# Optimization experiments

Measured on AMD Instinct MI355X. Metric: run time of the kernel, lower is better.

Reference implementation:

```python
import jax, jax.numpy as jnp
import numpy as np
from jax import lax

BETA = 0.1

def setup_inputs() -> dict:
    key = jax.random.key(0)
    k = jax.random.split(key, 6)
    B, T, H, V = 2, 1024, 1024, 64000
    return {
        "_input": jax.random.normal(k[0], (B, T, H), jnp.float32) * 0.02,
        "weight": jax.random.normal(k[1], (V, H), jnp.float32) * 0.02,
        "attention_mask": (jax.random.uniform(k[2], (B, T)) < 0.9).astype(jnp.float32),
        "rewards": jax.random.normal(k[3], (B,), jnp.float32),
        "ref_input": jax.random.normal(k[4], (B, T, H), jnp.float32) * 0.02,
        "ref_weight": jax.random.normal(k[5], (V, H), jnp.float32) * 0.02,
    }


def _grpo(log_probs, attention_mask, rewards, ref_log_probs, beta):
    # log_probs: [B,T,V]
    chosen = jnp.argmax(log_probs, axis=-1)  # [B,T] int
    tok_lp = jnp.take_along_axis(log_probs, chosen[..., None], axis=-1)[..., 0]  # [B,T]
    ref_tok_lp = lax.stop_gradient(
        jnp.take_along_axis(ref_log_probs, chosen[..., None], axis=-1)[..., 0]
    )
    adv = (rewards - rewards.mean()) / (jnp.std(rewards, ddof=1) + 1e-8)  # [B]
    ratio = jnp.exp(tok_lp - lax.stop_gradient(tok_lp))  # == 1 in fwd, grad-carrying
    policy_loss = -ratio * adv[:, None]
    d = ref_tok_lp - tok_lp
    kl = jnp.exp(d) - d - 1.0
    per_tok = (policy_loss + beta * kl) * attention_mask
    seqlen = jnp.clip(attention_mask.sum(axis=1), 1.0)
    loss = (per_tok.sum(axis=1) / seqlen).mean()
    metrics = (
        tok_lp.mean(),
        jnp.std(tok_lp, ddof=1),
        log_probs.mean(),
        (kl * attention_mask).sum(axis=1).mean() / attention_mask.sum(axis=1).mean(),
    )
    return loss, metrics


def reference(_input, weight, attention_mask, rewards, ref_input, ref_weight):
    logits = jnp.einsum("bth,vh->btv", _input, weight)
    log_probs = jax.nn.log_softmax(logits, axis=-1)
    ref_logits = jnp.einsum("bth,vh->btv", ref_input, ref_weight)
    ref_log_probs = lax.stop_gradient(jax.nn.log_softmax(ref_logits, axis=-1))
    loss, metrics = _grpo(log_probs, attention_mask, rewards, ref_log_probs, BETA)
    return (loss, *metrics)
```

## Files before the change

kernel.cpp:

```cpp
#include <hip/hip_runtime.h>
#include <math.h>

#define GRPO_BETA 0.1f

constexpr int BM = 128;
constexpr int BN = 256;
constexpr int BK = 32;

typedef __attribute__((ext_vector_type(4))) float   f32x4;
typedef __attribute__((ext_vector_type(8))) __bf16  bf16x8;

__device__ __forceinline__ float sexp_fast(float a) { return __expf(fminf(a, 0.f)); }
__device__ __forceinline__ float sexp(float a)      { return expf(fminf(a, 0.f)); }

__device__ __forceinline__ bf16x8 cvt8(float4 a, float4 b) {
  bf16x8 r;
  r[0] = (__bf16)a.x; r[1] = (__bf16)a.y; r[2] = (__bf16)a.z; r[3] = (__bf16)a.w;
  r[4] = (__bf16)b.x; r[5] = (__bf16)b.y; r[6] = (__bf16)b.z; r[7] = (__bf16)b.w;
  return r;
}

__device__ __forceinline__ void bar_lgkm() {
  asm volatile("s_waitcnt lgkmcnt(0)\n\ts_barrier" ::: "memory");
}

template <bool POLICY>
__global__ __launch_bounds__(512, 4)
void mfma_gemm_reduce(const float* __restrict__ A,
                      const float* __restrict__ W,
                      float* __restrict__ part,
                      int M, int K, int V, int NC, int NL, int gx)
{
  __shared__ __align__(16) unsigned short lds_a[BM * 64];
  __shared__ __align__(16) unsigned short lds_w[BN * 64];
  __shared__ __align__(16) float4 lds_red[BM * 4];

  const int tid  = threadIdx.x;
  const int lane = tid & 63;
  const int wave = tid >> 6;
  const int wm   = wave >> 2;
  const int wn   = wave & 3;
  const int l15  = lane & 15;
  const int q    = lane >> 4;

  const int nb  = gridDim.x;
  int wl = blockIdx.x;
  if ((nb & 7) == 0) wl = (wl & 7) * (nb >> 3) + (wl >> 3);
  const int bx    = wl % gx;
  const int chunk = wl / gx;
  const int row0  = bx * BM;

  const int t3 = tid & 3;
  const int r4 = tid >> 2;
  const int stw = ((t3 * 16) ^ ((r4 & 7) << 4));
  const int sta = r4 * 128 + stw;

  const int arow = min(row0 + r4, M - 1);
  const int aro  = arow * K + t3 * 8;

  const int swzr  = ((q * 16) ^ ((l15 & 7) << 4));
  const int aoff0 = (wm * 64 + l15) * 128 + swzr;
  const int woff0 = (wn * 64 + l15) * 128 + swzr;

  float rm = -INFINITY, rse = 0.f, rsum = 0.f;
  int   ridx = 0x7fffffff;

  const int NS = K / BK;

  for (int sub = 0; sub < NL; ++sub) {
    const int v0 = (chunk * NL + sub) * BN;
    if (v0 >= V) break;

    int wro[2];
#pragma unroll
    for (int i = 0; i < 2; ++i)
      wro[i] = min(v0 + r4 + 128 * i, V - 1) * K + t3 * 8;

    f32x4 acc[4][4];
#pragma unroll
    for (int i = 0; i < 4; ++i)
#pragma unroll
      for (int j = 0; j < 4; ++j) acc[i][j] = (f32x4){0.f, 0.f, 0.f, 0.f};

    float4 aA[2], wW[2][2];
    aA[0] = *reinterpret_cast<const float4*>(A + aro);
    aA[1] = *reinterpret_cast<const float4*>(A + aro + 4);
#pragma unroll
    for (int i = 0; i < 2; ++i) {
      wW[i][0] = *reinterpret_cast<const float4*>(W + wro[i]);
      wW[i][1] = *reinterpret_cast<const float4*>(W + wro[i] + 4);
    }
    *reinterpret_cast<bf16x8*>(reinterpret_cast<char*>(lds_a) + sta) = cvt8(aA[0], aA[1]);
#pragma unroll
    for (int i = 0; i < 2; ++i)
      *reinterpret_cast<bf16x8*>(reinterpret_cast<char*>(lds_w) + (r4 + 128 * i) * 128 + stw) =
          cvt8(wW[i][0], wW[i][1]);
    if (NS > 1) {
      aA[0] = *reinterpret_cast<const float4*>(A + aro + BK);
      aA[1] = *reinterpret_cast<const float4*>(A + aro + BK + 4);
#pragma unroll
      for (int i = 0; i < 2; ++i) {
        wW[i][0] = *reinterpret_cast<const float4*>(W + wro[i] + BK);
        wW[i][1] = *reinterpret_cast<const float4*>(W + wro[i] + BK + 4);
      }
    }
    bar_lgkm();

    for (int s = 0; s < NS; ++s) {
      const int p = (s & 1) << 6;

      bf16x8 afr[4];
#pragma unroll
      for (int f = 0; f < 4; ++f)
        afr[f] = *reinterpret_cast<const bf16x8*>(
            reinterpret_cast<const char*>(lds_a) + (aoff0 ^ p) + f * 2048);
      __builtin_amdgcn_s_setprio(1);
#pragma unroll
      for (int fn = 0; fn < 4; ++fn) {
        bf16x8 wfr = *reinterpret_cast<const bf16x8*>(
            reinterpret_cast<const char*>(lds_w) + (woff0 ^ p) + fn * 2048);
#pragma unroll
        for (int fm = 0; fm < 4; ++fm)
          acc[fm][fn] = __builtin_amdgcn_mfma_f32_16x16x32_bf16(
              afr[fm], wfr, acc[fm][fn], 0, 0, 0);
      }
      __builtin_amdgcn_s_setprio(0);

      if (s + 1 < NS) {
        const int p1 = ((s + 1) & 1) << 6;
        *reinterpret_cast<bf16x8*>(reinterpret_cast<char*>(lds_a) + (sta ^ p1)) =
            cvt8(aA[0], aA[1]);
#pragma unroll
        for (int i = 0; i < 2; ++i)
          *reinterpret_cast<bf16x8*>(
              reinterpret_cast<char*>(lds_w) + (((r4 + 128 * i) * 128 + stw) ^ p1)) =
              cvt8(wW[i][0], wW[i][1]);
        if (s + 2 < NS) {
          const int kf = (s + 2) * BK;
          aA[0] = *reinterpret_cast<const float4*>(A + aro + kf);
          aA[1] = *reinterpret_cast<const float4*>(A + aro + kf + 4);
#pragma unroll
          for (int i = 0; i < 2; ++i) {
            wW[i][0] = *reinterpret_cast<const float4*>(W + wro[i] + kf);
            wW[i][1] = *reinterpret_cast<const float4*>(W + wro[i] + kf + 4);
          }
        }
      }
      bar_lgkm();
    }

#pragma unroll
    for (int fm = 0; fm < 4; ++fm) {
#pragma unroll
      for (int reg = 0; reg < 4; ++reg) {
        float lm = -INFINITY;
#pragma unroll
        for (int fn = 0; fn < 4; ++fn) {
          const int v = v0 + wn * 64 + fn * 16 + l15;
          if (v < V) lm = fmaxf(lm, acc[fm][fn][reg]);
        }
#pragma unroll
        for (int d = 1; d < 16; d <<= 1) lm = fmaxf(lm, __shfl_xor(lm, d));
        float se = 0.f, sm = 0.f; int li = 0x7fffffff;
#pragma unroll
        for (int fn = 0; fn < 4; ++fn) {
          const int v = v0 + wn * 64 + fn * 16 + l15;
          if (v < V) {
            const float x = acc[fm][fn][reg];
            se += __expf(x - lm);
            sm += x;
            if (x == lm) li = min(li, v);
          }
        }
#pragma unroll
        for (int d = 1; d < 16; d <<= 1) {
          se += __shfl_xor(se, d);
          sm += __shfl_xor(sm, d);
          li  = min(li, __shfl_xor(li, d));
        }
        if (l15 == 0) {
          const int row = wm * 64 + fm * 16 + q * 4 + reg;
          lds_red[row * 4 + wn] = make_float4(lm, se, sm, __int_as_float(li));
        }
      }
    }
    __syncthreads();

    if (tid < BM) {
      float4 p = lds_red[tid * 4];
      float m = p.x, se = p.y, sm = p.z; int idx = __float_as_int(p.w);
#pragma unroll
      for (int j = 1; j < 4; ++j) {
        const float4 t = lds_red[tid * 4 + j];
        const int ti = __float_as_int(t.w);
        const float nm = fmaxf(m, t.x);
        se = se * sexp_fast(m - nm) + t.y * sexp_fast(t.x - nm);
        sm += t.z;
        if (t.x > m || (t.x == m && ti < idx)) idx = ti;
        m = nm;
      }
      const float nm = fmaxf(rm, m);
      rse = rse * sexp_fast(rm - nm) + se * sexp_fast(m - nm);
      rsum += sm;
      if (m > rm || (m == rm && idx < ridx)) ridx = idx;
      rm = nm;
    }
    __syncthreads();
  }

  if (tid < BM) {
    const int row = row0 + tid;
    if (row < M) {
      if (POLICY) {
        reinterpret_cast<float4*>(part)[(size_t)row * NC + chunk] =
            make_float4(rm, rse, rsum, __int_as_float(ridx));
      } else {
        reinterpret_cast<float2*>(part)[(size_t)row * NC + chunk] =
            make_float2(rm, rse);
      }
    }
  }
}

__global__ __launch_bounds__(256)
void combine_kernel(const float4* __restrict__ partP,
                    const float2* __restrict__ partR,
                    const float* __restrict__ refA,
                    const float* __restrict__ refW,
                    float4* __restrict__ rowtab,
                    int M, int K, int V, int NC)
{
  const int row = blockIdx.x;
  const int tid = threadIdx.x;

  __shared__ float redf[256];
  __shared__ int   redi[256];
  __shared__ float s_M, s_SE, s_SUM, s_Mr, s_SEr, s_dot;
  __shared__ int   s_idx;

  float m = -INFINITY, se = 0.f, sm = 0.f; int idx = 0x7fffffff;
  for (int i = tid; i < NC; i += 256) {
    float4 p = partP[(size_t)row * NC + i];
    int pi = __float_as_int(p.w);
    float nm = fmaxf(m, p.x);
    se = se * sexp(m - nm) + p.y * sexp(p.x - nm);
    if (p.x > m || (p.x == m && pi < idx)) idx = pi;
    m = nm;
    sm += p.z;
  }
  redf[tid] = m; redi[tid] = idx;
  __syncthreads();
  for (int s = 128; s > 0; s >>= 1) {
    if (tid < s) {
      float om = redf[tid + s]; int oi = redi[tid + s];
      if (om > redf[tid] || (om == redf[tid] && oi < redi[tid])) { redf[tid] = om; redi[tid] = oi; }
    }
    __syncthreads();
  }
  if (tid == 0) { s_M = redf[0]; s_idx = redi[0]; }
  __syncthreads();
  const float Mp = s_M; const int chosen = s_idx;

  float contrib = se * sexp(m - Mp);
  __syncthreads();
  redf[tid] = contrib; __syncthreads();
  for (int s = 128; s > 0; s >>= 1) { if (tid < s) redf[tid] += redf[tid + s]; __syncthreads(); }
  if (tid == 0) s_SE = redf[0];
  __syncthreads();
  redf[tid] = sm; __syncthreads();
  for (int s = 128; s > 0; s >>= 1) { if (tid < s) redf[tid] += redf[tid + s]; __syncthreads(); }
  if (tid == 0) s_SUM = redf[0];
  __syncthreads();

  float mr = -INFINITY, ser = 0.f;
  for (int i = tid; i < NC; i += 256) {
    float2 p = partR[(size_t)row * NC + i];
    float nm = fmaxf(mr, p.x);
    ser = ser * sexp(mr - nm) + p.y * sexp(p.x - nm);
    mr = nm;
  }
  redf[tid] = mr; __syncthreads();
  for (int s = 128; s > 0; s >>= 1) { if (tid < s) redf[tid] = fmaxf(redf[tid], redf[tid + s]); __syncthreads(); }
  if (tid == 0) s_Mr = redf[0];
  __syncthreads();
  const float Mr = s_Mr;
  float contribr = ser * sexp(mr - Mr);
  __syncthreads();
  redf[tid] = contribr; __syncthreads();
  for (int s = 128; s > 0; s >>= 1) { if (tid < s) redf[tid] += redf[tid + s]; __syncthreads(); }
  if (tid == 0) s_SEr = redf[0];
  __syncthreads();

  float dp = 0.f;
  const float* ar = refA + (size_t)row * K;
  const float* wr = refW + (size_t)chosen * K;
  for (int j = tid * 4; j < K; j += 256 * 4) {
    float4 x = *reinterpret_cast<const float4*>(ar + j);
    float4 y = *reinterpret_cast<const float4*>(wr + j);
    dp = fmaf(x.x, y.x, dp);
    dp = fmaf(x.y, y.y, dp);
    dp = fmaf(x.z, y.z, dp);
    dp = fmaf(x.w, y.w, dp);
  }
  __syncthreads();
  redf[tid] = dp; __syncthreads();
  for (int s = 128; s > 0; s >>= 1) { if (tid < s) redf[tid] += redf[tid + s]; __syncthreads(); }
  if (tid == 0) s_dot = redf[0];
  __syncthreads();

  if (tid == 0) {
    float lse     = Mp + logf(s_SE);
    float tok     = Mp - lse;
    float ref_lse = Mr + logf(s_SEr);
    float ref_tok = s_dot - ref_lse;
    float d  = ref_tok - tok;
    float kl = expm1f(d) - d;
    float rm3 = s_SUM / (float)V - lse;
    rowtab[row] = make_float4(tok, kl, rm3, 0.f);
  }
}

__global__ __launch_bounds__(256)
void final_kernel(const float4* __restrict__ rowtab,
                  const float* __restrict__ mask,
                  const float* __restrict__ rewards,
                  float* __restrict__ out,
                  int M, int B, int T)
{
  const int tid = threadIdx.x;
  __shared__ float redf[256];
  __shared__ float s_mean, s_m3, s_var;
  __shared__ float s_kl[16], s_cnt[16];

  float st = 0.f, sm3 = 0.f;
  for (int r = tid; r < M; r += 256) {
    float4 v = rowtab[r];
    st += v.x; sm3 += v.z;
  }
  redf[tid] = st; __syncthreads();
  for (int s = 128; s > 0; s >>= 1) { if (tid < s) redf[tid] += redf[tid + s]; __syncthreads(); }
  if (tid == 0) s_mean = redf[0] / (float)M;
  __syncthreads();
  redf[tid] = sm3; __syncthreads();
  for (int s = 128; s > 0; s >>= 1) { if (tid < s) redf[tid] += redf[tid + s]; __syncthreads(); }
  if (tid == 0) s_m3 = redf[0] / (float)M;
  __syncthreads();

  const float mean = s_mean;
  float sv = 0.f;
  for (int r = tid; r < M; r += 256) { float d = rowtab[r].x - mean; sv = fmaf(d, d, sv); }
  __syncthreads();
  redf[tid] = sv; __syncthreads();
  for (int s = 128; s > 0; s >>= 1) { if (tid < s) redf[tid] += redf[tid + s]; __syncthreads(); }
  if (tid == 0) s_var = redf[0];
  __syncthreads();

  const int nb = B < 16 ? B : 16;
  for (int b = 0; b < nb; ++b) {
    float lk = 0.f, lc = 0.f;
    for (int t = tid; t < T; t += 256) {
      int r = b * T + t;
      float mk = mask[r];
      lk = fmaf(rowtab[r].y, mk, lk);
      lc += mk;
    }
    __syncthreads();
    redf[tid] = lk; __syncthreads();
    for (int s = 128; s > 0; s >>= 1) { if (tid < s) redf[tid] += redf[tid + s]; __syncthreads(); }
    if (tid == 0) s_kl[b] = redf[0];
    __syncthreads();
    redf[tid] = lc; __syncthreads();
    for (int s = 128; s > 0; s >>= 1) { if (tid < s) redf[tid] += redf[tid + s]; __syncthreads(); }
    if (tid == 0) s_cnt[b] = redf[0];
    __syncthreads();
  }

  if (tid == 0) {
    float rmean = 0.f;
    for (int b = 0; b < B; ++b) rmean += rewards[b];
    rmean /= (float)B;
    float rv = 0.f;
    for (int b = 0; b < B; ++b) { float d = rewards[b] - rmean; rv += d * d; }
    float rstd = sqrtf(rv / (float)(B > 1 ? B - 1 : 1));

    float loss = 0.f, m4n = 0.f, m4d = 0.f;
    for (int b = 0; b < nb; ++b) {
      float adv  = (rewards[b] - rmean) / (rstd + 1e-8f);
      float cnt  = s_cnt[b];
      float seql = fmaxf(cnt, 1.0f);
      loss += (-adv * cnt + GRPO_BETA * s_kl[b]) / seql;
      m4n += s_kl[b];
      m4d += cnt;
    }
    loss /= (float)B;

    out[0] = loss;
    out[1] = s_mean;
    out[2] = sqrtf(s_var / (float)(M - 1));
    out[3] = s_m3;
    out[4] = m4n / m4d;
  }
}

extern "C" void kernel_launch(void* const* d_in, const int* in_sizes, int n_in,
                              void* d_out, int out_size, void* d_ws, size_t ws_size,
                              hipStream_t stream)
{
  if (n_in < 6) return;
  const float* A       = (const float*)d_in[0];
  const float* W       = (const float*)d_in[1];
  const float* mask    = (const float*)d_in[2];
  const float* rewards = (const float*)d_in[3];
  const float* rA      = (const float*)d_in[4];
  const float* rW      = (const float*)d_in[5];

  const int M = in_sizes[2];
  const int B = in_sizes[3];
  const int T = M / B;
  const int K = in_sizes[0] / M;
  const int V = in_sizes[1] / K;

  int NL = 1;
  auto need = [&](int nl) -> size_t {
    int nc = (V + BN * nl - 1) / (BN * nl);
    return (size_t)M * nc * 16 + (size_t)M * nc * 8 + (size_t)M * 16;
  };
  while (need(NL) > ws_size && NL < 1024) NL <<= 1;
  const int NC = (V + BN * NL - 1) / (BN * NL);
  const int gx = (M + BM - 1) / BM;

  float* partP  = (float*)d_ws;
  float* partR  = partP + (size_t)M * NC * 4;
  float* rowtab = partR + (size_t)M * NC * 2;

  dim3 g1(gx * NC), b1(512);
  mfma_gemm_reduce<true ><<<g1, b1, 0, stream>>>(A,  W,  partP, M, K, V, NC, NL, gx);
  mfma_gemm_reduce<false><<<g1, b1, 0, stream>>>(rA, rW, partR, M, K, V, NC, NL, gx);
  combine_kernel<<<dim3(M), dim3(256), 0, stream>>>(
      (const float4*)partP, (const float2*)partR, rA, rW, (float4*)rowtab, M, K, V, NC);
  final_kernel<<<dim3(1), dim3(256), 0, stream>>>(
      (const float4*)rowtab, mask, rewards, (float*)d_out, M, B, T);
}
```

Before: 911.6 us.

## Pre-convert activations and weights to bf16 before the GEMM-reduce kernels

Adds a grid-stride conversion kernel that writes bf16 copies of both inputs and both weight matrices into the workspace, when it is large enough. The GEMM kernels then load bf16 directly instead of re-reading fp32 and converting on every tile. This halves the global bytes each tile pulls in and removes conversion ALU work from the main loop. In exchange it adds four extra passes over the fp32 data (about 530 MB read, 265 MB written) and requires a much larger workspace; otherwise it falls back to the old path.

```diff
diff --git a/kernel.cpp b/kernel.cpp
--- a/kernel.cpp
+++ b/kernel.cpp
@@ -24,10 +24,25 @@
   asm volatile("s_waitcnt lgkmcnt(0)\n\ts_barrier" ::: "memory");
 }
 
-template <bool POLICY>
+__global__ __launch_bounds__(256)
+void cvt_bf16_kernel(const float* __restrict__ src, __bf16* __restrict__ dst,
+                     long long n8)
+{
+  long long i = (long long)blockIdx.x * blockDim.x + threadIdx.x;
+  const long long stride = (long long)gridDim.x * blockDim.x;
+  for (; i < n8; i += stride) {
+    const float4 a = *reinterpret_cast<const float4*>(src + i * 8);
+    const float4 b = *reinterpret_cast<const float4*>(src + i * 8 + 4);
+    *reinterpret_cast<bf16x8*>(dst + i * 8) = cvt8(a, b);
+  }
+}
+
+template <bool POLICY, bool CVT>
 __global__ __launch_bounds__(512, 4)
-void mfma_gemm_reduce(const float* __restrict__ A,
-                      const float* __restrict__ W,
+void mfma_gemm_reduce(const float* __restrict__ Af,
+                      const __bf16* __restrict__ Ah,
+                      const float* __restrict__ Wf,
+                      const __bf16* __restrict__ Wh,
                       float* __restrict__ part,
                       int M, int K, int V, int NC, int NL, int gx)
 {
@@ -82,26 +97,45 @@
 #pragma unroll
       for (int j = 0; j < 4; ++j) acc[i][j] = (f32x4){0.f, 0.f, 0.f, 0.f};
 
-    float4 aA[2], wW[2][2];
-    aA[0] = *reinterpret_cast<const float4*>(A + aro);
-    aA[1] = *reinterpret_cast<const float4*>(A + aro + 4);
-#pragma unroll
-    for (int i = 0; i < 2; ++i) {
-      wW[i][0] = *reinterpret_cast<const float4*>(W + wro[i]);
-      wW[i][1] = *reinterpret_cast<const float4*>(W + wro[i] + 4);
-    }
-    *reinterpret_cast<bf16x8*>(reinterpret_cast<char*>(lds_a) + sta) = cvt8(aA[0], aA[1]);
-#pragma unroll
-    for (int i = 0; i < 2; ++i)
-      *reinterpret_cast<bf16x8*>(reinterpret_cast<char*>(lds_w) + (r4 + 128 * i) * 128 + stw) =
-          cvt8(wW[i][0], wW[i][1]);
-    if (NS > 1) {
-      aA[0] = *reinterpret_cast<const float4*>(A + aro + BK);
-      aA[1] = *reinterpret_cast<const float4*>(A + aro + BK + 4);
+    float4 aF[2], wF[2][2];
+    bf16x8 aH, wH[2];
+
+    if constexpr (CVT) {
+      aF[0] = *reinterpret_cast<const float4*>(Af + aro);
+      aF[1] = *reinterpret_cast<const float4*>(Af + aro + 4);
 #pragma unroll
       for (int i = 0; i < 2; ++i) {
-        wW[i][0] = *reinterpret_cast<const float4*>(W + wro[i] + BK);
-        wW[i][1] = *reinterpret_cast<const float4*>(W + wro[i] + BK + 4);
+        wF[i][0] = *reinterpret_cast<const float4*>(Wf + wro[i]);
+        wF[i][1] = *reinterpret_cast<const float4*>(Wf + wro[i] + 4);
+      }
+      *reinterpret_cast<bf16x8*>(reinterpret_cast<char*>(lds_a) + sta) = cvt8(aF[0], aF[1]);
+#pragma unroll
+      for (int i = 0; i < 2; ++i)
+        *reinterpret_cast<bf16x8*>(reinterpret_cast<char*>(lds_w) + (r4 + 128 * i) * 128 + stw) =
+            cvt8(wF[i][0], wF[i][1]);
+      if (NS > 1) {
+        aF[0] = *reinterpret_cast<const float4*>(Af + aro + BK);
+        aF[1] = *reinterpret_cast<const float4*>(Af + aro + BK + 4);
+#pragma unroll
+        for (int i = 0; i < 2; ++i) {
+          wF[i][0] = *reinterpret_cast<const float4*>(Wf + wro[i] + BK);
+          wF[i][1] = *reinterpret_cast<const float4*>(Wf + wro[i] + BK + 4);
+        }
+      }
+    } else {
+      aH = *reinterpret_cast<const bf16x8*>(Ah + aro);
+#pragma unroll
+      for (int i = 0; i < 2; ++i)
+        wH[i] = *reinterpret_cast<const bf16x8*>(Wh + wro[i]);
+      *reinterpret_cast<bf16x8*>(reinterpret_cast<char*>(lds_a) + sta) = aH;
+#pragma unroll
+      for (int i = 0; i < 2; ++i)
+        *reinterpret_cast<bf16x8*>(reinterpret_cast<char*>(lds_w) + (r4 + 128 * i) * 128 + stw) = wH[i];
+      if (NS > 1) {
+        aH = *reinterpret_cast<const bf16x8*>(Ah + aro + BK);
+#pragma unroll
+        for (int i = 0; i < 2; ++i)
+          wH[i] = *reinterpret_cast<const bf16x8*>(Wh + wro[i] + BK);
       }
     }
     bar_lgkm();
@@ -128,21 +162,36 @@
 
       if (s + 1 < NS) {
         const int p1 = ((s + 1) & 1) << 6;
-        *reinterpret_cast<bf16x8*>(reinterpret_cast<char*>(lds_a) + (sta ^ p1)) =
-            cvt8(aA[0], aA[1]);
-#pragma unroll
-        for (int i = 0; i < 2; ++i)
-          *reinterpret_cast<bf16x8*>(
-              reinterpret_cast<char*>(lds_w) + (((r4 + 128 * i) * 128 + stw) ^ p1)) =
-              cvt8(wW[i][0], wW[i][1]);
-        if (s + 2 < NS) {
-          const int kf = (s + 2) * BK;
-          aA[0] = *reinterpret_cast<const float4*>(A + aro + kf);
-          aA[1] = *reinterpret_cast<const float4*>(A + aro + kf + 4);
-#pragma unroll
-          for (int i = 0; i < 2; ++i) {
-            wW[i][0] = *reinterpret_cast<const float4*>(W + wro[i] + kf);
-            wW[i][1] = *reinterpret_cast<const float4*>(W + wro[i] + kf + 4);
+        if constexpr (CVT) {
+          *reinterpret_cast<bf16x8*>(reinterpret_cast<char*>(lds_a) + (sta ^ p1)) =
+              cvt8(aF[0], aF[1]);
+#pragma unroll
+          for (int i = 0; i < 2; ++i)
+            *reinterpret_cast<bf16x8*>(
+                reinterpret_cast<char*>(lds_w) + (((r4 + 128 * i) * 128 + stw) ^ p1)) =
+                cvt8(wF[i][0], wF[i][1]);
+          if (s + 2 < NS) {
+            const int kf = (s + 2) * BK;
+            aF[0] = *reinterpret_cast<const float4*>(Af + aro + kf);
+            aF[1] = *reinterpret_cast<const float4*>(Af + aro + kf + 4);
+#pragma unroll
+            for (int i = 0; i < 2; ++i) {
+              wF[i][0] = *reinterpret_cast<const float4*>(Wf + wro[i] + kf);
+              wF[i][1] = *reinterpret_cast<const float4*>(Wf + wro[i] + kf + 4);
+            }
+          }
+        } else {
+          *reinterpret_cast<bf16x8*>(reinterpret_cast<char*>(lds_a) + (sta ^ p1)) = aH;
+#pragma unroll
+          for (int i = 0; i < 2; ++i)
+            *reinterpret_cast<bf16x8*>(
+                reinterpret_cast<char*>(lds_w) + (((r4 + 128 * i) * 128 + stw) ^ p1)) = wH[i];
+          if (s + 2 < NS) {
+            const int kf = (s + 2) * BK;
+            aH = *reinterpret_cast<const bf16x8*>(Ah + aro + kf);
+#pragma unroll
+            for (int i = 0; i < 2; ++i)
+              wH[i] = *reinterpret_cast<const bf16x8*>(Wh + wro[i] + kf);
           }
         }
       }
@@ -420,22 +469,53 @@
   const int K = in_sizes[0] / M;
   const int V = in_sizes[1] / K;
 
-  int NL = 1;
-  auto need = [&](int nl) -> size_t {
+  const int gx = (M + BM - 1) / BM;
+
+  const size_t aBytes = (size_t)M * K * sizeof(__bf16);
+  const size_t wBytes = (size_t)V * K * sizeof(__bf16);
+  auto partBytes = [&](int nl) -> size_t {
     int nc = (V + BN * nl - 1) / (BN * nl);
     return (size_t)M * nc * 16 + (size_t)M * nc * 8 + (size_t)M * 16;
   };
-  while (need(NL) > ws_size && NL < 1024) NL <<= 1;
+  const bool canPrep =
+      (K % 8 == 0) && (partBytes(1) + 2 * aBytes + 2 * wBytes <= ws_size);
+
+  int NL = 1;
+  if (!canPrep) {
+    while (partBytes(NL) > ws_size && NL < 1024) NL <<= 1;
+  }
   const int NC = (V + BN * NL - 1) / (BN * NL);
-  const int gx = (M + BM - 1) / BM;
 
   float* partP  = (float*)d_ws;
   float* partR  = partP + (size_t)M * NC * 4;
   float* rowtab = partR + (size_t)M * NC * 2;
 
   dim3 g1(gx * NC), b1(512);
-  mfma_gemm_reduce<true ><<<g1, b1, 0, stream>>>(A,  W,  partP, M, K, V, NC, NL, gx);
-  mfma_gemm_reduce<false><<<g1, b1, 0, stream>>>(rA, rW, partR, M, K, V, NC, NL, gx);
+
+  if (canPrep) {
+    __bf16* Ab  = (__bf16*)(rowtab + (size_t)M * 4);
+    __bf16* rAb = Ab  + (size_t)M * K;
+    __bf16* Wb  = rAb + (size_t)M * K;
+    __bf16* rWb = Wb  + (size_t)V * K;
+
+    const long long nA8 = (long long)M * K / 8;
+    const long long nW8 = (long long)V * K / 8;
+    cvt_bf16_kernel<<<dim3(512),  dim3(256), 0, stream>>>(A,  Ab,  nA8);
+    cvt_bf16_kernel<<<dim3(512),  dim3(256), 0, stream>>>(rA, rAb, nA8);
+    cvt_bf16_kernel<<<dim3(2048), dim3(256), 0, stream>>>(W,  Wb,  nW8);
+    cvt_bf16_kernel<<<dim3(2048), dim3(256), 0, stream>>>(rW, rWb, nW8);
+
+    mfma_gemm_reduce<true , false><<<g1, b1, 0, stream>>>(
+        nullptr, Ab,  nullptr, Wb,  partP, M, K, V, NC, NL, gx);
+    mfma_gemm_reduce<false, false><<<g1, b1, 0, stream>>>(
+        nullptr, rAb, nullptr, rWb, partR, M, K, V, NC, NL, gx);
+  } else {
+    mfma_gemm_reduce<true , true><<<g1, b1, 0, stream>>>(
+        A,  nullptr, W,  nullptr, partP, M, K, V, NC, NL, gx);
+    mfma_gemm_reduce<false, true><<<g1, b1, 0, stream>>>(
+        rA, nullptr, rW, nullptr, partR, M, K, V, NC, NL, gx);
+  }
+
   combine_kernel<<<dim3(M), dim3(256), 0, stream>>>(
       (const float4*)partP, (const float2*)partR, rA, rW, (float4*)rowtab, M, K, V, NC);
   final_kernel<<<dim3(1), dim3(256), 0, stream>>>(
```

After: 876.4 us. 3.9% less time.
